# Optimization experiments

Measured on AMD Instinct MI355X. Metric: run time of the kernel, lower is better.

The kernel has to match this reference:

```python
import jax, jax.numpy as jnp
import numpy as np

H = 16      # num_attention_heads
D = 64      # attention_head_size
HID = H * D # hidden_size = 1024
N = 1024    # seq_len == max_len
K = 1024    # position_buckets == att_span (K >= N so un-clamped indices stay in range)
EPS = 1e-7  # layer_norm_eps


def setup_inputs() -> dict:
    key = jax.random.key(0)
    ks = jax.random.split(key, 12)

    def w(k, shape):
        return jax.random.normal(k, shape, dtype=jnp.float32) * 0.02

    return {
        "hidden_states": jax.random.normal(ks[0], (1, N, HID), dtype=jnp.float32),
        "rel_embeddings": jax.random.normal(ks[1], (2 * K, HID), dtype=jnp.float32),
        "Wq": w(ks[2], (HID, HID)), "bq": jnp.zeros((HID,), jnp.float32),
        "Wk": w(ks[3], (HID, HID)), "bk": jnp.zeros((HID,), jnp.float32),
        "Wv": w(ks[4], (HID, HID)), "bv": jnp.zeros((HID,), jnp.float32),
        "Wpk": w(ks[5], (HID, HID)), "bpk": jnp.zeros((HID,), jnp.float32),
        "Wpq": w(ks[6], (HID, HID)), "bpq": jnp.zeros((HID,), jnp.float32),
        "Wo": w(ks[7], (HID, HID)), "bo": jnp.zeros((HID,), jnp.float32),
        "ln_g": jnp.ones((HID,), jnp.float32),
        "ln_b": jnp.zeros((HID,), jnp.float32),
    }


def _heads(x):
    # (L, HID) -> (H, L, D)   (batch size is 1, matching the baked-in id offsets)
    L = x.shape[0]
    return x.reshape(L, H, D).transpose(1, 0, 2)


def reference(hidden_states, rel_embeddings, Wq, bq, Wk, bk, Wv, bv,
              Wpk, bpk, Wpq, bpq, Wo, bo, ln_g, ln_b):
    hs = hidden_states[0]                       # (N, HID)
    q = _heads(hs @ Wq.T + bq)                  # (H, N, D)
    k = _heads(hs @ Wk.T + bk)                  # (H, N, D)
    v = _heads(hs @ Wv.T + bv)                  # (H, N, D)

    scale = jnp.sqrt(jnp.asarray(D * 3, jnp.float32))  # scale_factor = 1 + c2p + p2c = 3
    scores = jnp.einsum('hid,hjd->hij', q, k) / scale  # (H, N, N)

    pos_k = _heads(rel_embeddings @ Wpk.T + bpk)       # (H, 2K, D)
    pos_q = _heads(rel_embeddings @ Wpq.T + bpq)       # (H, 2K, D)

    rows = jnp.arange(N)[:, None]                      # (N, 1)
    # ids[i, j] = (i - j) + K  (no clamp in the original; valid since K >= N)
    idx = K + jnp.arange(N)[:, None] - jnp.arange(N)[None, :]  # (N, N)

    # c2p: gather c2p_att[h, i, K + i - j]
    c2p_att = jnp.einsum('hid,hkd->hik', q, pos_k)     # (H, N, 2K)
    c2p = c2p_att[:, rows, idx]                        # (H, N, N)

    # p2c: gather p2c_att[h, i, K + j - i], then transpose last two dims
    p2c_att = jnp.einsum('hid,hkd->hik', k, pos_q)     # (H, N, 2K)
    p2c = jnp.swapaxes(p2c_att[:, rows, idx.T], -1, -2)  # (H, N, N)

    scores = scores + (c2p + p2c) / scale
    attn = jax.nn.softmax(scores, axis=-1)             # (H, N, N)

    ctx = jnp.einsum('hij,hjd->hid', attn, v)          # (H, N, D)
    ctx = ctx.transpose(1, 0, 2).reshape(1, N, HID)    # (1, N, HID)

    # DebertaV2SelfOutput: dense + residual LayerNorm
    out = ctx @ Wo.T + bo
    x = out + hidden_states
    mu = jnp.mean(x, axis=-1, keepdims=True)
    var = jnp.mean(jnp.square(x - mu), axis=-1, keepdims=True)
    return ((x - mu) / jnp.sqrt(var + EPS)) * ln_g + ln_b
```

## Files before the change

kernel.cpp:

```cpp
#include <hip/hip_runtime.h>
#include <stdint.h>

#define HID 1024
#define NSEQ 1024
#define KREL 1024
#define NHEAD 16
#define DHEAD 64

typedef __attribute__((ext_vector_type(8))) short bhalf8;
typedef __attribute__((ext_vector_type(4))) float floatx4;

__device__ inline uint16_t f2bf(float f) {
  union { float f; uint32_t u; } c; c.f = f;
  uint32_t u = c.u;
  return (uint16_t)((u + 0x7fffu + ((u >> 16) & 1u)) >> 16);
}
__device__ inline uint32_t pkbf(float a, float b) {
  union { float f; uint32_t u; } x, y; x.f = a; y.f = b;
#if __has_builtin(__builtin_amdgcn_perm)
  return __builtin_amdgcn_perm(x.u + 0x8000u, y.u + 0x8000u, 0x03020706u);
#else
  return ((x.u + 0x8000u) >> 16) | ((y.u + 0x8000u) & 0xffff0000u);
#endif
}
__device__ inline void gl_lds16(const uint16_t* g, uint16_t* l) {
  __builtin_amdgcn_global_load_lds(
      (const __attribute__((address_space(1))) void*)g,
      (__attribute__((address_space(3))) void*)l, 16, 0, 0);
}

struct Cast8 {
  const float* src[8];
  uint16_t* dst[8];
  int n[8];
};
__global__ __launch_bounds__(256) void cast8_kernel(Cast8 c) {
  int seg = blockIdx.y;
  int n = c.n[seg];
  const float* s = c.src[seg];
  uint16_t* d = c.dst[seg];
  for (int idx = (blockIdx.x * 256 + threadIdx.x) * 4; idx < n; idx += 1024 * 256 * 4) {
    float4 v = *(const float4*)(s + idx);
    ushort4 o;
    o.x = f2bf(v.x); o.y = f2bf(v.y); o.z = f2bf(v.z); o.w = f2bf(v.w);
    *(ushort4*)(d + idx) = o;
  }
}

struct ProjArgs {
  const uint16_t* A[5];
  const uint16_t* W[5];
  const float* bias[5];
  uint16_t* C[5];
  int trans[5];
};
__global__ __launch_bounds__(256) void proj_gemm(ProjArgs pa) {
  __shared__ uint16_t a_s[2][4096];
  __shared__ uint16_t b_s[2][4096];
  int bidx = blockIdx.x;
  int xcd = bidx & 7, idx = bidx >> 3;
  int g = xcd * 7 + (idx >> 3);
  int nt = idx & 7;
  int z, mt;
  if (g < 24) { z = g >> 3; mt = g & 7; }
  else { int g2 = g - 24; z = 3 + (g2 >> 4); mt = g2 & 15; }
  const uint16_t* A = pa.A[z];
  const uint16_t* W = pa.W[z];
  int i0 = mt * 128, n0 = nt * 128;

  int t = threadIdx.x;
  int lane = t & 63, w = t >> 6;
  int fm = lane & 15, kq = lane >> 4;
  int wm = (w >> 1) * 64, wn = (w & 1) * 64;

  int sA = w * 2;
  const uint16_t* gA0 = A + (size_t)(i0 + sA * 16 + fm) * HID + kq * 8;
  const uint16_t* gB0 = W + (size_t)(n0 + sA * 16 + fm) * HID + kq * 8;

  floatx4 acc[4][4] = {};

  gl_lds16(gA0, &a_s[0][sA * 512]);
  gl_lds16(gA0 + 16 * HID, &a_s[0][(sA + 1) * 512]);
  gl_lds16(gB0, &b_s[0][sA * 512]);
  gl_lds16(gB0 + 16 * HID, &b_s[0][(sA + 1) * 512]);
  __syncthreads();

  int la = lane * 8;
  for (int kt = 0; kt < 32; ++kt) {
    int cur = kt & 1;
    if (kt < 31) {
      int ko = (kt + 1) * 32;
      gl_lds16(gA0 + ko, &a_s[cur ^ 1][sA * 512]);
      gl_lds16(gA0 + 16 * HID + ko, &a_s[cur ^ 1][(sA + 1) * 512]);
      gl_lds16(gB0 + ko, &b_s[cur ^ 1][sA * 512]);
      gl_lds16(gB0 + 16 * HID + ko, &b_s[cur ^ 1][(sA + 1) * 512]);
    }
    bhalf8 af[4], bf[4];
#pragma unroll
    for (int m2 = 0; m2 < 4; ++m2)
      af[m2] = *(bhalf8*)(&a_s[cur][((w >> 1) * 4 + m2) * 512 + la]);
#pragma unroll
    for (int n2 = 0; n2 < 4; ++n2)
      bf[n2] = *(bhalf8*)(&b_s[cur][((w & 1) * 4 + n2) * 512 + la]);
#pragma unroll
    for (int m2 = 0; m2 < 4; ++m2)
#pragma unroll
      for (int n2 = 0; n2 < 4; ++n2)
        acc[m2][n2] = __builtin_amdgcn_mfma_f32_16x16x32_bf16(af[m2], bf[n2], acc[m2][n2], 0, 0, 0);
    __syncthreads();
  }

  const float* bias = pa.bias[z];
  uint16_t* C = pa.C[z];
  int tr = pa.trans[z];
#pragma unroll
  for (int m2 = 0; m2 < 4; ++m2) {
    int rowb = i0 + wm + m2 * 16 + kq * 4;
#pragma unroll
    for (int n2 = 0; n2 < 4; ++n2) {
      int col = n0 + wn + n2 * 16 + fm;
      float bv = bias[col];
      floatx4 v = acc[m2][n2];
      if (tr) {
        uint2 p = { pkbf(v[0] + bv, v[1] + bv), pkbf(v[2] + bv, v[3] + bv) };
        *(uint2*)(C + (size_t)col * NSEQ + rowb) = p;
      } else {
#pragma unroll
        for (int r = 0; r < 4; ++r)
          C[(size_t)(rowb + r) * HID + col] = f2bf(v[r] + bv);
      }
    }
  }
}

__global__ __launch_bounds__(256) void out_gemm(const uint16_t* __restrict__ Abf,
                                                const uint16_t* __restrict__ W,
                                                const float* __restrict__ bias,
                                                float* __restrict__ C) {
  __shared__ uint16_t a_s[2][64 * 40];
  __shared__ uint16_t b_s[2][64 * 40];
  int bidx = blockIdx.x;
  int i0 = (bidx >> 4) * 64, n0 = (bidx & 15) * 64;
  int t = threadIdx.x;
  int lane = t & 63, w = t >> 6;
  int fm = lane & 15, kq = lane >> 4;
  int wm = (w >> 1) * 32, wn = (w & 1) * 32;
  int ra = t >> 2, ca = (t & 3) * 8;
  const uint16_t* Ap = Abf + (size_t)(i0 + ra) * HID + ca;
  const uint16_t* Wp = W + (size_t)(n0 + ra) * HID + ca;
  floatx4 acc00 = {0,0,0,0}, acc01 = {0,0,0,0}, acc10 = {0,0,0,0}, acc11 = {0,0,0,0};
  uint4 ua = *(const uint4*)(Ap);
  uint4 ub = *(const uint4*)(Wp);
  *(uint4*)(&a_s[0][ra * 40 + ca]) = ua;
  *(uint4*)(&b_s[0][ra * 40 + ca]) = ub;
  for (int kt = 0; kt < 32; ++kt) {
    __syncthreads();
    int cur = kt & 1;
    if (kt < 31) {
      int ko = (kt + 1) * 32;
      ua = *(const uint4*)(Ap + ko);
      ub = *(const uint4*)(Wp + ko);
    }
    const uint16_t* as = &a_s[cur][0];
    const uint16_t* bs = &b_s[cur][0];
    bhalf8 a0 = *(bhalf8*)(as + (wm + fm) * 40 + kq * 8);
    bhalf8 a1 = *(bhalf8*)(as + (wm + 16 + fm) * 40 + kq * 8);
    bhalf8 b0 = *(bhalf8*)(bs + (wn + fm) * 40 + kq * 8);
    bhalf8 b1 = *(bhalf8*)(bs + (wn + 16 + fm) * 40 + kq * 8);
    acc00 = __builtin_amdgcn_mfma_f32_16x16x32_bf16(a0, b0, acc00, 0, 0, 0);
    acc01 = __builtin_amdgcn_mfma_f32_16x16x32_bf16(a0, b1, acc01, 0, 0, 0);
    acc10 = __builtin_amdgcn_mfma_f32_16x16x32_bf16(a1, b0, acc10, 0, 0, 0);
    acc11 = __builtin_amdgcn_mfma_f32_16x16x32_bf16(a1, b1, acc11, 0, 0, 0);
    if (kt < 31) {
      int nxt = cur ^ 1;
      *(uint4*)(&a_s[nxt][ra * 40 + ca]) = ua;
      *(uint4*)(&b_s[nxt][ra * 40 + ca]) = ub;
    }
  }
  int rb0 = kq * 4;
#define EPO(ACC, SM, SN)                                                   \
  {                                                                        \
    int rowb = i0 + wm + (SM)*16 + rb0;                                    \
    int col = n0 + wn + (SN)*16 + fm;                                      \
    float bv_ = bias[col];                                                 \
    _Pragma("unroll")                                                      \
    for (int rr = 0; rr < 4; ++rr)                                         \
      C[(size_t)(rowb + rr) * HID + col] = ACC[rr] + bv_;                  \
  }
  EPO(acc00, 0, 0) EPO(acc01, 0, 1) EPO(acc10, 1, 0) EPO(acc11, 1, 1)
#undef EPO
}

__global__ __launch_bounds__(256) void attn_kernel(const uint16_t* __restrict__ qg,
                                                   const uint16_t* __restrict__ kg,
                                                   const uint16_t* __restrict__ vtg,
                                                   const uint16_t* __restrict__ pkg,
                                                   const uint16_t* __restrict__ pqg,
                                                   uint16_t* __restrict__ ctx) {
  const float RSCALE = 0.07216878364870323f;
  __shared__ uint16_t Qs[32][72];
  __shared__ uint16_t Ks[32][72];
  __shared__ uint16_t Vt[64][40];
  __shared__ uint16_t PKw[64][72];
  __shared__ uint16_t PQw[64][72];
  __shared__ float C2P[32][68];
  __shared__ float P2C[32][68];
  __shared__ float Sqk[32][36];
  __shared__ uint16_t Pbf[32][40];
  __shared__ float m_sm[32], l_sm[32], al_sm[32];

  int t = threadIdx.x;
  int lane = t & 63, w = t >> 6;
  int fm = lane & 15;
  int kq = lane >> 4;

  int b = blockIdx.x;
  int xcd = b & 7, slot = b >> 3;
  int h = xcd * 2 + (slot & 1);
  int i0 = (slot >> 1) * 32;
  int cb = h * DHEAD;

  {
    int r = t >> 3, chq = (t & 7) * 8;
    *(uint4*)(&Qs[r][chq]) = *(const uint4*)(qg + (size_t)(i0 + r) * HID + cb + chq);
  }
  if (t < 32) { m_sm[t] = -1e30f; l_sm[t] = 0.f; }

  floatx4 opv0 = {0,0,0,0}, opv1 = {0,0,0,0};
  int wn = w * 16;
  int smt = w >> 1, snt = w & 1;
  int i2 = t >> 3, jj = t & 7;

  int pr = t >> 3, pch = (t & 7) * 8;
  int rV = t >> 2, cV = (t & 3) * 8;
  const uint16_t* kb = kg + cb + pch;
  const uint16_t* vb = vtg + (size_t)(cb + rV) * HID + cV;
  const uint16_t* pkb = pkg + cb + pch;
  const uint16_t* pqb = pqg + cb + pch;

  uint4 rk, rv, rpk0, rpk1, rpq0, rpq1;
  {
    int j0 = 0;
    int rbase = KREL + i0 - j0 - 31;
    rk = *(const uint4*)(kb + (size_t)(j0 + pr) * HID);
    rv = *(const uint4*)(vb + j0);
    int rg0 = rbase + pr;
    int rg1 = rbase + pr + 32; if (rg1 > 2047) rg1 = 2047;
    rpk0 = *(const uint4*)(pkb + (size_t)rg0 * HID);
    rpk1 = *(const uint4*)(pkb + (size_t)rg1 * HID);
    rpq0 = *(const uint4*)(pqb + (size_t)rg0 * HID);
    rpq1 = *(const uint4*)(pqb + (size_t)rg1 * HID);
  }

  for (int jt = 0; jt < NSEQ / 32; ++jt) {
    __syncthreads();
    *(uint4*)(&Ks[pr][pch]) = rk;
    *(uint4*)(&Vt[rV][cV]) = rv;
    *(uint4*)(&PKw[pr][pch]) = rpk0;
    *(uint4*)(&PKw[pr + 32][pch]) = rpk1;
    *(uint4*)(&PQw[pr][pch]) = rpq0;
    *(uint4*)(&PQw[pr + 32][pch]) = rpq1;
    __syncthreads();

    if (jt + 1 < NSEQ / 32) {
      int j0 = (jt + 1) * 32;
      int rbase = KREL + i0 - j0 - 31;
      rk = *(const uint4*)(kb + (size_t)(j0 + pr) * HID);
      rv = *(const uint4*)(vb + j0);
      int rg0 = rbase + pr; if (rg0 < 0) rg0 = 0;
      int rg1 = rbase + pr + 32; if (rg1 > 2047) rg1 = 2047;
      rpk0 = *(const uint4*)(pkb + (size_t)rg0 * HID);
      rpk1 = *(const uint4*)(pkb + (size_t)rg1 * HID);
      rpq0 = *(const uint4*)(pqb + (size_t)rg0 * HID);
      rpq1 = *(const uint4*)(pqb + (size_t)rg1 * HID);
    }

    {
      const uint16_t* Asrc = (w < 2) ? &Qs[0][0] : &Ks[0][0];
      const uint16_t* Bsrc = (w < 2) ? &PKw[0][0] : &PQw[0][0];
      float* Cdst = (w < 2) ? &C2P[0][0] : &P2C[0][0];
      int ntb = (w & 1) * 2;
#pragma unroll
      for (int mt = 0; mt < 2; ++mt) {
        bhalf8 a0 = *(bhalf8*)(Asrc + (mt * 16 + fm) * 72 + kq * 8);
        bhalf8 a1 = *(bhalf8*)(Asrc + (mt * 16 + fm) * 72 + kq * 8 + 32);
#pragma unroll
        for (int nt = ntb; nt < ntb + 2; ++nt) {
          bhalf8 b0 = *(bhalf8*)(Bsrc + (nt * 16 + fm) * 72 + kq * 8);
          bhalf8 b1 = *(bhalf8*)(Bsrc + (nt * 16 + fm) * 72 + kq * 8 + 32);
          floatx4 acc = {0,0,0,0};
          acc = __builtin_amdgcn_mfma_f32_16x16x32_bf16(a0, b0, acc, 0, 0, 0);
          acc = __builtin_amdgcn_mfma_f32_16x16x32_bf16(a1, b1, acc, 0, 0, 0);
#pragma unroll
          for (int r = 0; r < 4; ++r)
            Cdst[(mt * 16 + kq * 4 + r) * 68 + nt * 16 + fm] = acc[r];
        }
      }
      bhalf8 qa0 = *(bhalf8*)(&Qs[smt * 16 + fm][kq * 8]);
      bhalf8 qa1 = *(bhalf8*)(&Qs[smt * 16 + fm][kq * 8 + 32]);
      bhalf8 kb0 = *(bhalf8*)(&Ks[snt * 16 + fm][kq * 8]);
      bhalf8 kb1 = *(bhalf8*)(&Ks[snt * 16 + fm][kq * 8 + 32]);
      floatx4 sacc = {0,0,0,0};
      sacc = __builtin_amdgcn_mfma_f32_16x16x32_bf16(qa0, kb0, sacc, 0, 0, 0);
      sacc = __builtin_amdgcn_mfma_f32_16x16x32_bf16(qa1, kb1, sacc, 0, 0, 0);
#pragma unroll
      for (int r = 0; r < 4; ++r)
        Sqk[smt * 16 + kq * 4 + r][snt * 16 + fm] = sacc[r];
    }
    __syncthreads();

    {
      float sv[4];
#pragma unroll
      for (int q = 0; q < 4; ++q) {
        int j = jj + 8 * q;
        int rr = i2 - j + 31;
        sv[q] = (Sqk[i2][j] + C2P[i2][rr] + P2C[j][rr]) * RSCALE;
      }
      float mx = fmaxf(fmaxf(sv[0], sv[1]), fmaxf(sv[2], sv[3]));
      mx = fmaxf(mx, __shfl_xor(mx, 1));
      mx = fmaxf(mx, __shfl_xor(mx, 2));
      mx = fmaxf(mx, __shfl_xor(mx, 4));
      float m_old = m_sm[i2];
      float m_new = fmaxf(m_old, mx);
      float al = __expf(m_old - m_new);
      float ts = 0.f;
#pragma unroll
      for (int q = 0; q < 4; ++q) {
        float e = __expf(sv[q] - m_new);
        Pbf[i2][jj + 8 * q] = f2bf(e);
        ts += e;
      }
      ts += __shfl_xor(ts, 1);
      ts += __shfl_xor(ts, 2);
      ts += __shfl_xor(ts, 4);
      if (jj == 0) { m_sm[i2] = m_new; l_sm[i2] = l_sm[i2] * al + ts; al_sm[i2] = al; }
    }
    __syncthreads();

    {
#pragma unroll
      for (int r = 0; r < 4; ++r) {
        opv0[r] *= al_sm[kq * 4 + r];
        opv1[r] *= al_sm[16 + kq * 4 + r];
      }
      bhalf8 vbf = *(bhalf8*)(&Vt[wn + fm][kq * 8]);
      bhalf8 pa0 = *(bhalf8*)(&Pbf[fm][kq * 8]);
      bhalf8 pa1 = *(bhalf8*)(&Pbf[16 + fm][kq * 8]);
      opv0 = __builtin_amdgcn_mfma_f32_16x16x32_bf16(pa0, vbf, opv0, 0, 0, 0);
      opv1 = __builtin_amdgcn_mfma_f32_16x16x32_bf16(pa1, vbf, opv1, 0, 0, 0);
    }
  }

#pragma unroll
  for (int r = 0; r < 4; ++r) {
    int ia = kq * 4 + r, ib = 16 + kq * 4 + r;
    float la = 1.0f / l_sm[ia], lb = 1.0f / l_sm[ib];
    ctx[(size_t)(i0 + ia) * HID + cb + wn + fm] = f2bf(opv0[r] * la);
    ctx[(size_t)(i0 + ib) * HID + cb + wn + fm] = f2bf(opv1[r] * lb);
  }
}

__global__ __launch_bounds__(256) void ln_kernel(const float* __restrict__ xin,
                                                 const float* __restrict__ hs,
                                                 const float* __restrict__ g,
                                                 const float* __restrict__ b,
                                                 float* __restrict__ y) {
  int row = blockIdx.x, t = threadIdx.x;
  int c = t * 4;
  float4 a = *(const float4*)(xin + (size_t)row * HID + c);
  float4 hv = *(const float4*)(hs + (size_t)row * HID + c);
  float x0 = a.x + hv.x, x1 = a.y + hv.y, x2 = a.z + hv.z, x3 = a.w + hv.w;
  float s = x0 + x1 + x2 + x3;
  float sq = x0 * x0 + x1 * x1 + x2 * x2 + x3 * x3;
  for (int off = 32; off; off >>= 1) {
    s += __shfl_xor(s, off);
    sq += __shfl_xor(sq, off);
  }
  __shared__ float rs[4], rq[4];
  int w = t >> 6, lane = t & 63;
  if (lane == 0) { rs[w] = s; rq[w] = sq; }
  __syncthreads();
  s = rs[0] + rs[1] + rs[2] + rs[3];
  sq = rq[0] + rq[1] + rq[2] + rq[3];
  float mu = s * (1.0f / HID);
  float var = sq * (1.0f / HID) - mu * mu;
  float rstd = rsqrtf(var + 1e-7f);
  float4 gg = *(const float4*)(g + c);
  float4 bb = *(const float4*)(b + c);
  float4 out;
  out.x = (x0 - mu) * rstd * gg.x + bb.x;
  out.y = (x1 - mu) * rstd * gg.y + bb.y;
  out.z = (x2 - mu) * rstd * gg.z + bb.z;
  out.w = (x3 - mu) * rstd * gg.w + bb.w;
  *(float4*)(y + (size_t)row * HID + c) = out;
}

extern "C" void kernel_launch(void* const* d_in, const int* in_sizes, int n_in,
                              void* d_out, int out_size, void* d_ws, size_t ws_size,
                              hipStream_t stream) {
  const float* hs  = (const float*)d_in[0];
  const float* rel = (const float*)d_in[1];
  const float* Wq  = (const float*)d_in[2];  const float* bq  = (const float*)d_in[3];
  const float* Wk  = (const float*)d_in[4];  const float* bk  = (const float*)d_in[5];
  const float* Wv  = (const float*)d_in[6];  const float* bv  = (const float*)d_in[7];
  const float* Wpk = (const float*)d_in[8];  const float* bpk = (const float*)d_in[9];
  const float* Wpq = (const float*)d_in[10]; const float* bpq = (const float*)d_in[11];
  const float* Wo  = (const float*)d_in[12]; const float* bo  = (const float*)d_in[13];
  const float* lng = (const float*)d_in[14]; const float* lnb = (const float*)d_in[15];

  char* ws = (char*)d_ws;
  const size_t MB = 1024 * 1024;
  uint16_t* q_bf   = (uint16_t*)(ws + 0 * MB);
  uint16_t* k_bf   = (uint16_t*)(ws + 2 * MB);
  uint16_t* vt_bf  = (uint16_t*)(ws + 4 * MB);
  uint16_t* pk_bf  = (uint16_t*)(ws + 6 * MB);
  uint16_t* pq_bf  = (uint16_t*)(ws + 10 * MB);
  uint16_t* ctx_bf = (uint16_t*)(ws + 14 * MB);
  float*    out_f  = (float*)   (ws + 16 * MB);
  uint16_t* hs_bf  = (uint16_t*)(ws + 20 * MB);
  uint16_t* rel_bf = (uint16_t*)(ws + 22 * MB);
  uint16_t* Wq_bf  = (uint16_t*)(ws + 26 * MB);
  uint16_t* Wk_bf  = (uint16_t*)(ws + 28 * MB);
  uint16_t* Wv_bf  = (uint16_t*)(ws + 30 * MB);
  uint16_t* Wpk_bf = (uint16_t*)(ws + 32 * MB);
  uint16_t* Wpq_bf = (uint16_t*)(ws + 34 * MB);
  uint16_t* Wo_bf  = (uint16_t*)(ws + 36 * MB);

  dim3 blk(256);

  Cast8 c8;
  c8.src[0] = hs;  c8.dst[0] = hs_bf;  c8.n[0] = 1024 * 1024;
  c8.src[1] = rel; c8.dst[1] = rel_bf; c8.n[1] = 2048 * 1024;
  c8.src[2] = Wq;  c8.dst[2] = Wq_bf;  c8.n[2] = 1024 * 1024;
  c8.src[3] = Wk;  c8.dst[3] = Wk_bf;  c8.n[3] = 1024 * 1024;
  c8.src[4] = Wv;  c8.dst[4] = Wv_bf;  c8.n[4] = 1024 * 1024;
  c8.src[5] = Wpk; c8.dst[5] = Wpk_bf; c8.n[5] = 1024 * 1024;
  c8.src[6] = Wpq; c8.dst[6] = Wpq_bf; c8.n[6] = 1024 * 1024;
  c8.src[7] = Wo;  c8.dst[7] = Wo_bf;  c8.n[7] = 1024 * 1024;
  cast8_kernel<<<dim3(1024, 8), blk, 0, stream>>>(c8);

  ProjArgs pa;
  pa.A[0] = hs_bf;  pa.A[1] = hs_bf;  pa.A[2] = hs_bf;  pa.A[3] = rel_bf; pa.A[4] = rel_bf;
  pa.W[0] = Wq_bf;  pa.W[1] = Wk_bf;  pa.W[2] = Wv_bf;  pa.W[3] = Wpk_bf; pa.W[4] = Wpq_bf;
  pa.bias[0] = bq;  pa.bias[1] = bk;  pa.bias[2] = bv;  pa.bias[3] = bpk; pa.bias[4] = bpq;
  pa.C[0] = q_bf; pa.C[1] = k_bf; pa.C[2] = vt_bf; pa.C[3] = pk_bf; pa.C[4] = pq_bf;
  pa.trans[0] = 0; pa.trans[1] = 0; pa.trans[2] = 1; pa.trans[3] = 0; pa.trans[4] = 0;
  proj_gemm<<<dim3(448), blk, 0, stream>>>(pa);

  attn_kernel<<<dim3(512), blk, 0, stream>>>(q_bf, k_bf, vt_bf, pk_bf, pq_bf, ctx_bf);

  out_gemm<<<dim3(256), blk, 0, stream>>>(ctx_bf, Wo_bf, bo, out_f);

  ln_kernel<<<dim3(1024), blk, 0, stream>>>(out_f, hs, lng, lnb, (float*)d_out);
}
```

Baseline: 216.5 us.

## Split attention over key halves with merge kernel; rework proj_gemm LDS loads

The attention kernel now splits each query block's key range into two halves. That doubles the grid to 1024 blocks, and each block writes unnormalized partial outputs plus its row max and row sum. A new merge kernel combines the two halves with log-sum-exp rescaling to produce the bf16 context. The projection GEMM drops the direct global-to-LDS loads in favour of register-staged loads into padded LDS rows (stride 40), with the store placed after the MFMAs. Q fragments are also kept in registers, and Q's LDS storage is aliased with C2P. In exchange there is an extra kernel launch and extra global traffic for the partial results, and the partials reuse workspace regions that held the already-consumed casted inputs.

```diff
diff --git a/kernel.cpp b/kernel.cpp
--- a/kernel.cpp
+++ b/kernel.cpp
@@ -22,11 +22,6 @@
 #else
   return ((x.u + 0x8000u) >> 16) | ((y.u + 0x8000u) & 0xffff0000u);
 #endif
-}
-__device__ inline void gl_lds16(const uint16_t* g, uint16_t* l) {
-  __builtin_amdgcn_global_load_lds(
-      (const __attribute__((address_space(1))) void*)g,
-      (__attribute__((address_space(3))) void*)l, 16, 0, 0);
 }
 
 struct Cast8 {
@@ -55,8 +50,8 @@
   int trans[5];
 };
 __global__ __launch_bounds__(256) void proj_gemm(ProjArgs pa) {
-  __shared__ uint16_t a_s[2][4096];
-  __shared__ uint16_t b_s[2][4096];
+  __shared__ uint16_t a_s[2][128 * 40];
+  __shared__ uint16_t b_s[2][128 * 40];
   int bidx = blockIdx.x;
   int xcd = bidx & 7, idx = bidx >> 3;
   int g = xcd * 7 + (idx >> 3);
@@ -73,41 +68,52 @@
   int fm = lane & 15, kq = lane >> 4;
   int wm = (w >> 1) * 64, wn = (w & 1) * 64;
 
-  int sA = w * 2;
-  const uint16_t* gA0 = A + (size_t)(i0 + sA * 16 + fm) * HID + kq * 8;
-  const uint16_t* gB0 = W + (size_t)(n0 + sA * 16 + fm) * HID + kq * 8;
+  int ra = t >> 1, ca = (t & 1) * 16;
+  const uint16_t* Ap = A + (size_t)(i0 + ra) * HID + ca;
+  const uint16_t* Wp = W + (size_t)(n0 + ra) * HID + ca;
 
   floatx4 acc[4][4] = {};
 
-  gl_lds16(gA0, &a_s[0][sA * 512]);
-  gl_lds16(gA0 + 16 * HID, &a_s[0][(sA + 1) * 512]);
-  gl_lds16(gB0, &b_s[0][sA * 512]);
-  gl_lds16(gB0 + 16 * HID, &b_s[0][(sA + 1) * 512]);
-  __syncthreads();
-
-  int la = lane * 8;
+  uint4 ua0 = *(const uint4*)(Ap);
+  uint4 ua1 = *(const uint4*)(Ap + 8);
+  uint4 ub0 = *(const uint4*)(Wp);
+  uint4 ub1 = *(const uint4*)(Wp + 8);
+  *(uint4*)(&a_s[0][ra * 40 + ca]) = ua0;
+  *(uint4*)(&a_s[0][ra * 40 + ca + 8]) = ua1;
+  *(uint4*)(&b_s[0][ra * 40 + ca]) = ub0;
+  *(uint4*)(&b_s[0][ra * 40 + ca + 8]) = ub1;
+
   for (int kt = 0; kt < 32; ++kt) {
+    __syncthreads();
     int cur = kt & 1;
     if (kt < 31) {
       int ko = (kt + 1) * 32;
-      gl_lds16(gA0 + ko, &a_s[cur ^ 1][sA * 512]);
-      gl_lds16(gA0 + 16 * HID + ko, &a_s[cur ^ 1][(sA + 1) * 512]);
-      gl_lds16(gB0 + ko, &b_s[cur ^ 1][sA * 512]);
-      gl_lds16(gB0 + 16 * HID + ko, &b_s[cur ^ 1][(sA + 1) * 512]);
-    }
+      ua0 = *(const uint4*)(Ap + ko);
+      ua1 = *(const uint4*)(Ap + ko + 8);
+      ub0 = *(const uint4*)(Wp + ko);
+      ub1 = *(const uint4*)(Wp + ko + 8);
+    }
+    const uint16_t* as = &a_s[cur][0];
+    const uint16_t* bs = &b_s[cur][0];
     bhalf8 af[4], bf[4];
 #pragma unroll
     for (int m2 = 0; m2 < 4; ++m2)
-      af[m2] = *(bhalf8*)(&a_s[cur][((w >> 1) * 4 + m2) * 512 + la]);
+      af[m2] = *(bhalf8*)(as + (wm + m2 * 16 + fm) * 40 + kq * 8);
 #pragma unroll
     for (int n2 = 0; n2 < 4; ++n2)
-      bf[n2] = *(bhalf8*)(&b_s[cur][((w & 1) * 4 + n2) * 512 + la]);
+      bf[n2] = *(bhalf8*)(bs + (wn + n2 * 16 + fm) * 40 + kq * 8);
 #pragma unroll
     for (int m2 = 0; m2 < 4; ++m2)
 #pragma unroll
       for (int n2 = 0; n2 < 4; ++n2)
         acc[m2][n2] = __builtin_amdgcn_mfma_f32_16x16x32_bf16(af[m2], bf[n2], acc[m2][n2], 0, 0, 0);
-    __syncthreads();
+    if (kt < 31) {
+      int nxt = cur ^ 1;
+      *(uint4*)(&a_s[nxt][ra * 40 + ca]) = ua0;
+      *(uint4*)(&a_s[nxt][ra * 40 + ca + 8]) = ua1;
+      *(uint4*)(&b_s[nxt][ra * 40 + ca]) = ub0;
+      *(uint4*)(&b_s[nxt][ra * 40 + ca + 8]) = ub1;
+    }
   }
 
   const float* bias = pa.bias[z];
@@ -196,14 +202,17 @@
                                                    const uint16_t* __restrict__ vtg,
                                                    const uint16_t* __restrict__ pkg,
                                                    const uint16_t* __restrict__ pqg,
-                                                   uint16_t* __restrict__ ctx) {
+                                                   float* __restrict__ Opart,
+                                                   float* __restrict__ mpart,
+                                                   float* __restrict__ lpart) {
   const float RSCALE = 0.07216878364870323f;
-  __shared__ uint16_t Qs[32][72];
+  __shared__ char QC2P[32 * 68 * 4];
+  uint16_t (*Qs)[72] = (uint16_t(*)[72])QC2P;
+  float (*C2P)[68] = (float(*)[68])QC2P;
   __shared__ uint16_t Ks[32][72];
   __shared__ uint16_t Vt[64][40];
   __shared__ uint16_t PKw[64][72];
   __shared__ uint16_t PQw[64][72];
-  __shared__ float C2P[32][68];
   __shared__ float P2C[32][68];
   __shared__ float Sqk[32][36];
   __shared__ uint16_t Pbf[32][40];
@@ -217,7 +226,9 @@
   int b = blockIdx.x;
   int xcd = b & 7, slot = b >> 3;
   int h = xcd * 2 + (slot & 1);
-  int i0 = (slot >> 1) * 32;
+  int s = (slot >> 1) & 1;
+  int ib = slot >> 2;
+  int i0 = ib * 32;
   int cb = h * DHEAD;
 
   {
@@ -225,6 +236,13 @@
     *(uint4*)(&Qs[r][chq]) = *(const uint4*)(qg + (size_t)(i0 + r) * HID + cb + chq);
   }
   if (t < 32) { m_sm[t] = -1e30f; l_sm[t] = 0.f; }
+  __syncthreads();
+  bhalf8 qf[2][2];
+#pragma unroll
+  for (int m2 = 0; m2 < 2; ++m2) {
+    qf[m2][0] = *(bhalf8*)(&Qs[m2 * 16 + fm][kq * 8]);
+    qf[m2][1] = *(bhalf8*)(&Qs[m2 * 16 + fm][kq * 8 + 32]);
+  }
 
   floatx4 opv0 = {0,0,0,0}, opv1 = {0,0,0,0};
   int wn = w * 16;
@@ -238,13 +256,14 @@
   const uint16_t* pkb = pkg + cb + pch;
   const uint16_t* pqb = pqg + cb + pch;
 
+  int jt_beg = s * 16, jt_end = s * 16 + 16;
   uint4 rk, rv, rpk0, rpk1, rpq0, rpq1;
   {
-    int j0 = 0;
+    int j0 = jt_beg * 32;
     int rbase = KREL + i0 - j0 - 31;
     rk = *(const uint4*)(kb + (size_t)(j0 + pr) * HID);
     rv = *(const uint4*)(vb + j0);
-    int rg0 = rbase + pr;
+    int rg0 = rbase + pr; if (rg0 < 0) rg0 = 0;
     int rg1 = rbase + pr + 32; if (rg1 > 2047) rg1 = 2047;
     rpk0 = *(const uint4*)(pkb + (size_t)rg0 * HID);
     rpk1 = *(const uint4*)(pkb + (size_t)rg1 * HID);
@@ -252,7 +271,7 @@
     rpq1 = *(const uint4*)(pqb + (size_t)rg1 * HID);
   }
 
-  for (int jt = 0; jt < NSEQ / 32; ++jt) {
+  for (int jt = jt_beg; jt < jt_end; ++jt) {
     __syncthreads();
     *(uint4*)(&Ks[pr][pch]) = rk;
     *(uint4*)(&Vt[rV][cV]) = rv;
@@ -262,7 +281,7 @@
     *(uint4*)(&PQw[pr + 32][pch]) = rpq1;
     __syncthreads();
 
-    if (jt + 1 < NSEQ / 32) {
+    if (jt + 1 < jt_end) {
       int j0 = (jt + 1) * 32;
       int rbase = KREL + i0 - j0 - 31;
       rk = *(const uint4*)(kb + (size_t)(j0 + pr) * HID);
@@ -276,14 +295,19 @@
     }
 
     {
-      const uint16_t* Asrc = (w < 2) ? &Qs[0][0] : &Ks[0][0];
       const uint16_t* Bsrc = (w < 2) ? &PKw[0][0] : &PQw[0][0];
       float* Cdst = (w < 2) ? &C2P[0][0] : &P2C[0][0];
       int ntb = (w & 1) * 2;
+      bhalf8 ka[2][2];
 #pragma unroll
       for (int mt = 0; mt < 2; ++mt) {
-        bhalf8 a0 = *(bhalf8*)(Asrc + (mt * 16 + fm) * 72 + kq * 8);
-        bhalf8 a1 = *(bhalf8*)(Asrc + (mt * 16 + fm) * 72 + kq * 8 + 32);
+        ka[mt][0] = *(bhalf8*)(&Ks[mt * 16 + fm][kq * 8]);
+        ka[mt][1] = *(bhalf8*)(&Ks[mt * 16 + fm][kq * 8 + 32]);
+      }
+#pragma unroll
+      for (int mt = 0; mt < 2; ++mt) {
+        bhalf8 a0 = (w < 2) ? qf[mt][0] : ka[mt][0];
+        bhalf8 a1 = (w < 2) ? qf[mt][1] : ka[mt][1];
 #pragma unroll
         for (int nt = ntb; nt < ntb + 2; ++nt) {
           bhalf8 b0 = *(bhalf8*)(Bsrc + (nt * 16 + fm) * 72 + kq * 8);
@@ -296,13 +320,9 @@
             Cdst[(mt * 16 + kq * 4 + r) * 68 + nt * 16 + fm] = acc[r];
         }
       }
-      bhalf8 qa0 = *(bhalf8*)(&Qs[smt * 16 + fm][kq * 8]);
-      bhalf8 qa1 = *(bhalf8*)(&Qs[smt * 16 + fm][kq * 8 + 32]);
-      bhalf8 kb0 = *(bhalf8*)(&Ks[snt * 16 + fm][kq * 8]);
-      bhalf8 kb1 = *(bhalf8*)(&Ks[snt * 16 + fm][kq * 8 + 32]);
       floatx4 sacc = {0,0,0,0};
-      sacc = __builtin_amdgcn_mfma_f32_16x16x32_bf16(qa0, kb0, sacc, 0, 0, 0);
-      sacc = __builtin_amdgcn_mfma_f32_16x16x32_bf16(qa1, kb1, sacc, 0, 0, 0);
+      sacc = __builtin_amdgcn_mfma_f32_16x16x32_bf16(qf[smt][0], ka[snt][0], sacc, 0, 0, 0);
+      sacc = __builtin_amdgcn_mfma_f32_16x16x32_bf16(qf[smt][1], ka[snt][1], sacc, 0, 0, 0);
 #pragma unroll
       for (int r = 0; r < 4; ++r)
         Sqk[smt * 16 + kq * 4 + r][snt * 16 + fm] = sacc[r];
@@ -352,13 +372,44 @@
     }
   }
 
+  int part = (h * 32 + ib) * 2 + s;
+  float* Op = Opart + (size_t)part * 2048;
 #pragma unroll
   for (int r = 0; r < 4; ++r) {
-    int ia = kq * 4 + r, ib = 16 + kq * 4 + r;
-    float la = 1.0f / l_sm[ia], lb = 1.0f / l_sm[ib];
-    ctx[(size_t)(i0 + ia) * HID + cb + wn + fm] = f2bf(opv0[r] * la);
-    ctx[(size_t)(i0 + ib) * HID + cb + wn + fm] = f2bf(opv1[r] * lb);
-  }
+    Op[(kq * 4 + r) * 64 + wn + fm] = opv0[r];
+    Op[(16 + kq * 4 + r) * 64 + wn + fm] = opv1[r];
+  }
+  if (t < 32) {
+    mpart[part * 32 + t] = m_sm[t];
+    lpart[part * 32 + t] = l_sm[t];
+  }
+}
+
+__global__ __launch_bounds__(256) void merge_kernel(const float* __restrict__ Opart,
+                                                    const float* __restrict__ mpart,
+                                                    const float* __restrict__ lpart,
+                                                    uint16_t* __restrict__ ctx) {
+  int blk = blockIdx.x;
+  int h = blk >> 5, ib = blk & 31;
+  int t = threadIdx.x;
+  int il = t >> 3, dc = (t & 7) * 8;
+  int p0 = (h * 32 + ib) * 2, p1 = p0 + 1;
+  float m1 = mpart[p0 * 32 + il], m2 = mpart[p1 * 32 + il];
+  float l1 = lpart[p0 * 32 + il], l2 = lpart[p1 * 32 + il];
+  float m = fmaxf(m1, m2);
+  float w1 = __expf(m1 - m), w2 = __expf(m2 - m);
+  float inv = 1.0f / (l1 * w1 + l2 * w2);
+  size_t o0 = (size_t)p0 * 2048 + il * 64 + dc;
+  float4 a0 = *(const float4*)(Opart + o0);
+  float4 a1 = *(const float4*)(Opart + o0 + 4);
+  float4 b0 = *(const float4*)(Opart + o0 + 2048);
+  float4 b1 = *(const float4*)(Opart + o0 + 2048 + 4);
+  uint4 u;
+  u.x = pkbf((a0.x * w1 + b0.x * w2) * inv, (a0.y * w1 + b0.y * w2) * inv);
+  u.y = pkbf((a0.z * w1 + b0.z * w2) * inv, (a0.w * w1 + b0.w * w2) * inv);
+  u.z = pkbf((a1.x * w1 + b1.x * w2) * inv, (a1.y * w1 + b1.y * w2) * inv);
+  u.w = pkbf((a1.z * w1 + b1.z * w2) * inv, (a1.w * w1 + b1.w * w2) * inv);
+  *(uint4*)(ctx + (size_t)(ib * 32 + il) * HID + h * 64 + dc) = u;
 }
 
 __global__ __launch_bounds__(256) void ln_kernel(const float* __restrict__ xin,
@@ -426,6 +477,9 @@
   uint16_t* Wpk_bf = (uint16_t*)(ws + 32 * MB);
   uint16_t* Wpq_bf = (uint16_t*)(ws + 34 * MB);
   uint16_t* Wo_bf  = (uint16_t*)(ws + 36 * MB);
+  float*    Opart  = (float*)   (ws + 20 * MB);
+  float*    mpart  = (float*)   (ws + 28 * MB);
+  float*    lpart  = (float*)   (ws + 28 * MB + 128 * 1024);
 
   dim3 blk(256);
 
@@ -448,7 +502,10 @@
   pa.trans[0] = 0; pa.trans[1] = 0; pa.trans[2] = 1; pa.trans[3] = 0; pa.trans[4] = 0;
   proj_gemm<<<dim3(448), blk, 0, stream>>>(pa);
 
-  attn_kernel<<<dim3(512), blk, 0, stream>>>(q_bf, k_bf, vt_bf, pk_bf, pq_bf, ctx_bf);
+  attn_kernel<<<dim3(1024), blk, 0, stream>>>(q_bf, k_bf, vt_bf, pk_bf, pq_bf,
+                                              Opart, mpart, lpart);
+
+  merge_kernel<<<dim3(512), blk, 0, stream>>>(Opart, mpart, lpart, ctx_bf);
 
   out_gemm<<<dim3(256), blk, 0, stream>>>(ctx_bf, Wo_bf, bo, out_f);
 
```

After: 279.5 us. +29.1%, slower.
